# Kernel tuning notes

Measured on AMD Instinct MI355X. Metric: run time of the kernel, lower is better.

## Reference

```python
import jax, jax.numpy as jnp
from jax import lax
import numpy as np

B, H, N, F = 8, 512, 64, 256
P = 12  # prediction_steps


def setup_inputs() -> dict:
    key = jax.random.key(0)
    ks = jax.random.split(key, 6)
    s_in = 1.0 / np.sqrt(N * F)
    s_f = 1.0 / np.sqrt(F)
    return {
        "x": jax.random.normal(ks[0], (B, H, N, F), jnp.float32),
        "W1": jax.random.normal(ks[1], (N * F, F), jnp.float32) * s_in,
        "b1": jnp.zeros((F,), jnp.float32),
        "Wx": jax.random.normal(ks[2], (F, 4 * F), jnp.float32) * s_f,
        "Wh": jax.random.normal(ks[3], (F, 4 * F), jnp.float32) * s_f,
        "b": jnp.zeros((4 * F,), jnp.float32),
        "Wa": jax.random.normal(ks[4], (F, F), jnp.float32) * s_f,
        "ba": jnp.zeros((F,), jnp.float32),
        "W2": jax.random.normal(ks[5], (F, N), jnp.float32) * s_f,
        "b2": jnp.zeros((N,), jnp.float32),
    }


def _lstm_cell(h, c, xt, Wx, Wh, b):
    # Keras LSTMCell gate order: i, f, g(candidate), o
    z = xt @ Wx + h @ Wh + b  # (B, 4F)
    i, f, g, o = jnp.split(z, 4, axis=-1)
    c_new = jax.nn.sigmoid(f) * c + jax.nn.sigmoid(i) * jnp.tanh(g)
    h_new = jax.nn.sigmoid(o) * jnp.tanh(c_new)
    return h_new, c_new


def reference(x, W1, b1, Wx, Wh, b, Wa, ba, W2, b2):
    Bx, Hx, Nx, Fx = x.shape
    xs = x.reshape(Bx, Hx, Nx * Fx) @ W1 + b1  # dense1: (B,H,F)

    def enc_step(carry, xt):
        h, c = carry
        h, c = _lstm_cell(h, c, xt, Wx, Wh, b)
        return (h, c), h

    h0 = jnp.zeros((Bx, Fx), x.dtype)
    (h, c), enc = lax.scan(enc_step, (h0, h0), jnp.swapaxes(xs, 0, 1))
    enc = jnp.swapaxes(enc, 0, 1)  # encoder_states (B,H,F)

    def dec_step(carry, _):
        h, c, mem = carry
        q = mem @ Wa + ba                          # (B,F)
        scores = jnp.einsum('bf,bhf->bh', q, enc)  # dot-product attention
        w = jax.nn.softmax(scores, axis=-1)
        ctx = jnp.einsum('bh,bhf->bf', w, enc)
        h, c = _lstm_cell(h, c, ctx, Wx, Wh, b)
        return (h, c, h), h

    (_, _, _), preds = lax.scan(dec_step, (h, c, h), None, length=P)
    preds = jnp.swapaxes(preds, 0, 1)  # (B,P,F)
    return preds @ W2 + b2  # (B,P,N)
```

## Files before the change

### kernel.cpp

```cpp
#include <hip/hip_runtime.h>
#include <hip/hip_bf16.h>
#include <stdint.h>

#define B_ 8
#define H_ 512
#define F_ 256
#define P_ 12
#define M_ 4096
#define K1_ 16384
#define J_ 1024

typedef __attribute__((ext_vector_type(8))) short short8;
typedef __attribute__((ext_vector_type(4))) float floatx4;

union FragU { uint4 u; short8 s; };

#define OFF_W1H   ((size_t)0)
#define OFF_W1L   ((size_t)8388608)
#define OFF_WHSW  ((size_t)16777216)
#define OFF_ENC   ((size_t)17301504)
#define OFF_C     ((size_t)21495808)
#define OFF_XSUM  ((size_t)21504000)
#define OFF_XPRE  ((size_t)25698304)
#define OFF_P1    ((size_t)42475520)
#define OFF_ENCT  (OFF_P1)
#define OFF_HST   (OFF_P1 + (size_t)4194304)
#define OFF_CTXG  (OFF_HST + (size_t)8192)
#define OFF_ZG    (OFF_CTXG + (size_t)8192)

__device__ __forceinline__ unsigned short f2bf(float f) {
  uint32_t u = __float_as_uint(f);
  u += 0x7fffu + ((u >> 16) & 1u);
  return (unsigned short)(u >> 16);
}
__device__ __forceinline__ float bf2f(unsigned short h) {
  return __uint_as_float(((uint32_t)h) << 16);
}
__device__ __forceinline__ float sigm(float x) { return 1.f / (1.f + __expf(-x)); }
__device__ __forceinline__ float tanh_(float x) {
  float ax = fabsf(x);
  float e  = __expf(-2.f * ax);
  float t  = (1.f - e) / (1.f + e);
  return x < 0.f ? -t : t;
}

__global__ void k_prep_w1(const float* __restrict__ W1,
                          uint4* __restrict__ hi, uint4* __restrict__ lo) {
  int idx  = blockIdx.x * 1024 + threadIdx.x;
  int lane = idx & 63;
  int kt   = (idx >> 6) & 511;
  int nt   = idx >> 15;
  int n    = nt * 16 + (lane & 15);
  int kb   = kt * 32 + ((lane >> 4) << 3);
  unsigned short h8[8], l8[8];
#pragma unroll
  for (int j = 0; j < 8; ++j) {
    float v = W1[(size_t)(kb + j) * 256 + n];
    unsigned short hh = f2bf(v);
    h8[j] = hh;
    l8[j] = f2bf(v - bf2f(hh));
  }
  uint4 uh, ul;
  uh.x = (uint32_t)h8[0] | ((uint32_t)h8[1] << 16);
  uh.y = (uint32_t)h8[2] | ((uint32_t)h8[3] << 16);
  uh.z = (uint32_t)h8[4] | ((uint32_t)h8[5] << 16);
  uh.w = (uint32_t)h8[6] | ((uint32_t)h8[7] << 16);
  ul.x = (uint32_t)l8[0] | ((uint32_t)l8[1] << 16);
  ul.y = (uint32_t)l8[2] | ((uint32_t)l8[3] << 16);
  ul.z = (uint32_t)l8[4] | ((uint32_t)l8[5] << 16);
  ul.w = (uint32_t)l8[6] | ((uint32_t)l8[7] << 16);
  hi[idx] = uh;
  lo[idx] = ul;
}

__global__ void k_prep_wh(const float* __restrict__ Wh, uint4* __restrict__ sw) {
  int idx  = blockIdx.x * 1024 + threadIdx.x;
  int lane = idx & 63;
  int kt   = (idx >> 6) & 7;
  int zt   = idx >> 9;
  int col  = zt * 16 + (lane & 15);
  int kb   = kt * 32 + ((lane >> 4) << 3);
  unsigned short h8[8];
#pragma unroll
  for (int j = 0; j < 8; ++j) h8[j] = f2bf(Wh[(size_t)(kb + j) * 1024 + col]);
  uint4 u;
  u.x = (uint32_t)h8[0] | ((uint32_t)h8[1] << 16);
  u.y = (uint32_t)h8[2] | ((uint32_t)h8[3] << 16);
  u.z = (uint32_t)h8[4] | ((uint32_t)h8[5] << 16);
  u.w = (uint32_t)h8[6] | ((uint32_t)h8[7] << 16);
  sw[idx] = u;
}

__global__ __launch_bounds__(1024)
void k_gemm1(const float* __restrict__ x, const uint4* __restrict__ w1h,
             const uint4* __restrict__ w1l, float* __restrict__ P1) {
  __shared__ __align__(16) unsigned short xh[128 * 40];
  __shared__ __align__(16) unsigned short xl[128 * 40];
  int bm = blockIdx.x >> 3, kc = blockIdx.x & 7;
  int m0 = bm * 128, kcbase = kc * 2048;
  int tid = threadIdx.x, wave = tid >> 6, lane = tid & 63;
  int quad = lane >> 4, l15 = lane & 15;
  int srow = tid >> 3, skch = tid & 7;
  floatx4 acc[8];
#pragma unroll
  for (int mt = 0; mt < 8; ++mt) acc[mt] = (floatx4)(0.f);

  const float* xrow = x + (size_t)(m0 + srow) * K1_ + kcbase + skch * 4;
  float4 xv = *(const float4*)(xrow);
  for (int it = 0; it < 64; ++it) {
    unsigned short h0 = f2bf(xv.x), h1 = f2bf(xv.y), h2 = f2bf(xv.z), h3 = f2bf(xv.w);
    unsigned short g0 = f2bf(xv.x - bf2f(h0)), g1 = f2bf(xv.y - bf2f(h1));
    unsigned short g2 = f2bf(xv.z - bf2f(h2)), g3 = f2bf(xv.w - bf2f(h3));
    uint2 ph, pl;
    ph.x = (uint32_t)h0 | ((uint32_t)h1 << 16); ph.y = (uint32_t)h2 | ((uint32_t)h3 << 16);
    pl.x = (uint32_t)g0 | ((uint32_t)g1 << 16); pl.y = (uint32_t)g2 | ((uint32_t)g3 << 16);
    *(uint2*)&xh[srow * 40 + skch * 4] = ph;
    *(uint2*)&xl[srow * 40 + skch * 4] = pl;
    __syncthreads();

    float4 xn = xv;
    if (it < 63) xn = *(const float4*)(xrow + (it + 1) * 32);

    size_t aoff = (size_t)(wave * 512 + kc * 64 + it) * 64 + lane;
    FragU ah; ah.u = w1h[aoff];
    FragU al; al.u = w1l[aoff];
#pragma unroll
    for (int mt = 0; mt < 8; ++mt) {
      FragU bh, bl;
      bh.u = *(const uint4*)&xh[(mt * 16 + l15) * 40 + quad * 8];
      bl.u = *(const uint4*)&xl[(mt * 16 + l15) * 40 + quad * 8];
      acc[mt] = __builtin_amdgcn_mfma_f32_16x16x32_bf16(ah.s, bh.s, acc[mt], 0, 0, 0);
      acc[mt] = __builtin_amdgcn_mfma_f32_16x16x32_bf16(ah.s, bl.s, acc[mt], 0, 0, 0);
      acc[mt] = __builtin_amdgcn_mfma_f32_16x16x32_bf16(al.s, bh.s, acc[mt], 0, 0, 0);
    }
    __syncthreads();
    xv = xn;
  }
  int nbase = wave * 16 + quad * 4;
#pragma unroll
  for (int mt = 0; mt < 8; ++mt) {
    int m = m0 + mt * 16 + l15;
#pragma unroll
    for (int r = 0; r < 4; ++r)
      P1[(size_t)(kc * 256 + nbase + r) * M_ + m] = acc[mt][r];
  }
}

__global__ void k_reduce(const float* __restrict__ P1, const float* __restrict__ b1,
                         float* __restrict__ xsum) {
  int idx = blockIdx.x * 1024 + threadIdx.x;
  int k = idx >> 12, m = idx & 4095;
  float s = b1[k];
#pragma unroll
  for (int kc = 0; kc < 8; ++kc) s += P1[(size_t)(kc * 256 + k) * M_ + m];
  xsum[(size_t)k * M_ + m] = s;
}

__global__ __launch_bounds__(256)
void k_gemm2(const float* __restrict__ xsum, const float* __restrict__ Wx,
             const float* __restrict__ bz, float* __restrict__ Xpre) {
  int m0 = blockIdx.x * 16;
  int j = threadIdx.x;
  float acc0[16], acc1[16], acc2[16], acc3[16];
  float bb0 = bz[j], bb1 = bz[256 + j], bb2 = bz[512 + j], bb3 = bz[768 + j];
#pragma unroll
  for (int mm = 0; mm < 16; ++mm) { acc0[mm] = bb0; acc1[mm] = bb1; acc2[mm] = bb2; acc3[mm] = bb3; }
#pragma unroll 4
  for (int k = 0; k < 256; ++k) {
    float w0 = Wx[(size_t)k * 1024 + j];
    float w1 = Wx[(size_t)k * 1024 + 256 + j];
    float w2 = Wx[(size_t)k * 1024 + 512 + j];
    float w3 = Wx[(size_t)k * 1024 + 768 + j];
#pragma unroll
    for (int mm = 0; mm < 16; ++mm) {
      float xv = xsum[(size_t)k * M_ + m0 + mm];
      acc0[mm] += xv * w0; acc1[mm] += xv * w1; acc2[mm] += xv * w2; acc3[mm] += xv * w3;
    }
  }
#pragma unroll
  for (int mm = 0; mm < 16; ++mm) {
    float* o = Xpre + (size_t)(m0 + mm) * 1024;
    o[j] = acc0[mm]; o[256 + j] = acc1[mm]; o[512 + j] = acc2[mm]; o[768 + j] = acc3[mm];
  }
}

__global__ __launch_bounds__(512, 2)
void k_encoder(const uint4* __restrict__ whsw, const float* __restrict__ Xpre,
               float* __restrict__ enc, float* __restrict__ encT,
               float* __restrict__ cws) {
  __shared__ uint4 wl[8192];
  __shared__ __align__(16) unsigned short hb[2][512];
  __shared__ __align__(16) float zsh[2048];
  int b = blockIdx.x, tid = threadIdx.x;
  int wave = tid >> 6, lane = tid & 63;
  int quad = lane >> 4, l15 = lane & 15;
  int e = tid & 1, j = tid >> 1;

  for (int r = 0; r < 16; ++r) {
    int u = r * 512 + tid;
    int ln = u & 63, fr = u >> 6;
    int w = fr >> 4, G = (fr >> 3) & 1, kt = fr & 7;
    int zt = 16 * (2 * G + 1) + 2 * w + 1;
    wl[u] = whsw[(size_t)((zt * 8 + kt) * 64 + ln)];
  }
  uint4 wfr[48];
#pragma unroll
  for (int G = 0; G < 2; ++G)
#pragma unroll
    for (int i = 0; i < 3; ++i) {
      int zt = 16 * (2 * G + (i >> 1)) + 2 * wave + (i & 1);
#pragma unroll
      for (int kt = 0; kt < 8; ++kt)
        wfr[(G * 3 + i) * 8 + kt] = whsw[(size_t)((zt * 8 + kt) * 64 + lane)];
    }

  hb[0][tid] = 0; hb[1][tid] = 0;
  float c_ = 0.f;
  const float* xpb = Xpre + (size_t)b * 512 * 1024;
  int colA = 256 * e + j;
  int colB = 512 + colA;
  int hoff  = ((l15 == 1) ? 256 : 0) + quad * 8;
  int zwoff = ((l15 == 1) ? 1024 : 0) + quad * 4;
  __syncthreads();

  int cur = 0;
  for (int t = 0; t < 512; ++t) {
    const unsigned short* hbc = hb[cur];
    float xA = xpb[(size_t)t * 1024 + colA];
    float xB = xpb[(size_t)t * 1024 + colB];

#pragma unroll
    for (int G = 0; G < 2; ++G) {
      const uint4* wlg = wl + (size_t)((wave * 2 + G) * 8) * 64 + lane;
      FragU bfr[8], pfr[8];
#pragma unroll
      for (int k = 0; k < 3; ++k) {
        bfr[k].u = *(const uint4*)&hbc[hoff + k * 32];
        pfr[k].u = wlg[(size_t)k * 64];
      }
      floatx4 a0 = (floatx4)(0.f), a1 = (floatx4)(0.f);
      floatx4 a2 = (floatx4)(0.f), a3 = (floatx4)(0.f);
#pragma unroll
      for (int kt = 0; kt < 8; ++kt) {
        if (kt < 5) {
          bfr[kt + 3].u = *(const uint4*)&hbc[hoff + (kt + 3) * 32];
          pfr[kt + 3].u = wlg[(size_t)(kt + 3) * 64];
        }
        FragU f0, f1, f2;
        f0.u = wfr[(G * 3 + 0) * 8 + kt];
        f1.u = wfr[(G * 3 + 1) * 8 + kt];
        f2.u = wfr[(G * 3 + 2) * 8 + kt];
        a0 = __builtin_amdgcn_mfma_f32_16x16x32_bf16(f0.s, bfr[kt].s, a0, 0, 0, 0);
        a1 = __builtin_amdgcn_mfma_f32_16x16x32_bf16(f1.s, bfr[kt].s, a1, 0, 0, 0);
        a2 = __builtin_amdgcn_mfma_f32_16x16x32_bf16(f2.s, bfr[kt].s, a2, 0, 0, 0);
        a3 = __builtin_amdgcn_mfma_f32_16x16x32_bf16(pfr[kt].s, bfr[kt].s, a3, 0, 0, 0);
      }
      if (l15 < 2) {
        int zt0 = 16 * (2 * G) + 2 * wave;
        int zt2 = 16 * (2 * G + 1) + 2 * wave;
        *(floatx4*)&zsh[zwoff + zt0 * 16]        = a0;
        *(floatx4*)&zsh[zwoff + (zt0 + 1) * 16]  = a1;
        *(floatx4*)&zsh[zwoff + zt2 * 16]        = a2;
        *(floatx4*)&zsh[zwoff + (zt2 + 1) * 16]  = a3;
      }
    }

    float zA = zsh[colA] + zsh[1024 + colA] + xA;
    float zB = zsh[colB] + zsh[1024 + colB] + xB;
    float actA = sigm(zA);
    float tnh = tanh_(zB), sg = sigm(zB);
    float actB = e ? sg : tnh;
    float p = actA * actB;
    float send = e ? actA : p;
    float recv = __shfl_xor(send, 1, 64);
    float cn = e ? (actA * c_ + recv)
                 : (recv * c_ + p);
    c_ = cn;
    float th = tanh_(cn);
    float hn = actB * th;
    int nxt = cur ^ 1;
    if (e) {
      enc[((size_t)b * 512 + t) * 256 + j] = hn;
      encT[((size_t)b * 256 + j) * 512 + t] = hn;
      unsigned short hh = f2bf(hn);
      hb[nxt][j] = hh;
      hb[nxt][256 + j] = f2bf(hn - bf2f(hh));
    }
    __syncthreads();
    cur = nxt;
  }
  if (e) cws[b * 256 + j] = c_;
}

__global__ __launch_bounds__(1024)
void k_dec_att(const float* __restrict__ enc, const float* __restrict__ encT,
               float* __restrict__ hst, float* __restrict__ cst,
               const float* __restrict__ zg, float* __restrict__ ctxg,
               const float* __restrict__ Wa, const float* __restrict__ ba,
               const float* __restrict__ W2, const float* __restrict__ b2,
               float* __restrict__ out, int p) {
  __shared__ float hsh[256], qsh[256], sc[512], smx[2];
  __shared__ float zb[1024];
  int b = blockIdx.x, tid = threadIdx.x;
  const float* encb = enc + (size_t)b * 512 * 256;

  if (p > 0) {
    if (tid < 256) {
      float zi = zg[b * 1024 + tid];
      float zf = zg[b * 1024 + 256 + tid];
      float zgg = zg[b * 1024 + 512 + tid];
      float zo = zg[b * 1024 + 768 + tid];
      float ig = sigm(zi), fg = sigm(zf), gg = tanh_(zgg), og = sigm(zo);
      float cn = fg * cst[b * 256 + tid] + ig * gg;
      cst[b * 256 + tid] = cn;
      float hn = og * tanh_(cn);
      hsh[tid] = hn;
      hst[b * 256 + tid] = hn;
    }
    __syncthreads();
    {
      if (tid < 512) {
        int col = tid & 63, kc = tid >> 6;
        float s = 0.f;
#pragma unroll
        for (int i = 0; i < 32; ++i) {
          int k = kc * 32 + i;
          s += hsh[k] * W2[(size_t)k * 64 + col];
        }
        zb[tid] = s;
      }
    }
    __syncthreads();
    if (tid < 64) {
      float s = b2[tid];
#pragma unroll
      for (int kc = 0; kc < 8; ++kc) s += zb[kc * 64 + tid];
      out[((size_t)b * 12 + (p - 1)) * 64 + tid] = s;
    }
  } else {
    if (tid < 256) {
      float hv = encb[(size_t)511 * 256 + tid];
      hsh[tid] = hv;
      hst[b * 256 + tid] = hv;
    }
  }
  if (p == 12) return;
  __syncthreads();

  {
    int j = tid & 255, kc = tid >> 8;
    float s = 0.f;
#pragma unroll 8
    for (int i = 0; i < 64; ++i) {
      int k = kc * 64 + i;
      s += hsh[k] * Wa[(size_t)k * 256 + j];
    }
    zb[tid] = s;
  }
  __syncthreads();
  if (tid < 256) qsh[tid] = ba[tid] + zb[tid] + zb[256 + tid] + zb[512 + tid] + zb[768 + tid];
  __syncthreads();

  {
    int hh = tid & 511, kc = tid >> 9;
    const float* eT = encT + (size_t)b * 256 * 512;
    float s = 0.f;
#pragma unroll 8
    for (int i = 0; i < 128; ++i) {
      int k = kc * 128 + i;
      s += qsh[k] * eT[(size_t)k * 512 + hh];
    }
    zb[tid] = s;
  }
  __syncthreads();
  if (tid < 512) sc[tid] = zb[tid] + zb[512 + tid];
  __syncthreads();

  if (tid < 64) {
    float m = -3.4e38f;
#pragma unroll
    for (int r = 0; r < 8; ++r) m = fmaxf(m, sc[tid * 8 + r]);
#pragma unroll
    for (int off = 32; off >= 1; off >>= 1) m = fmaxf(m, __shfl_xor(m, off, 64));
    if (tid == 0) smx[0] = m;
  }
  __syncthreads();
  if (tid < 512) sc[tid] = __expf(sc[tid] - smx[0]);
  __syncthreads();
  if (tid < 64) {
    float s = 0.f;
#pragma unroll
    for (int r = 0; r < 8; ++r) s += sc[tid * 8 + r];
#pragma unroll
    for (int off = 32; off >= 1; off >>= 1) s += __shfl_xor(s, off, 64);
    if (tid == 0) smx[1] = 1.f / s;
  }
  __syncthreads();

  {
    int j = tid & 255, hs = tid >> 8;
    float s = 0.f;
#pragma unroll 8
    for (int r = 0; r < 128; ++r) {
      int hh = hs * 128 + r;
      s += sc[hh] * encb[(size_t)hh * 256 + j];
    }
    zb[tid] = s;
  }
  __syncthreads();
  if (tid < 256)
    ctxg[b * 256 + tid] = (zb[tid] + zb[256 + tid] + zb[512 + tid] + zb[768 + tid]) * smx[1];
}

__global__ __launch_bounds__(512)
void k_dec_z(const float* __restrict__ ctxg, const float* __restrict__ hst,
             const float* __restrict__ Wx, const float* __restrict__ Wh,
             const float* __restrict__ bz, float* __restrict__ zg) {
  __shared__ float ldsx[256], ldsh[256], zsh[512];
  int chunk = blockIdx.x & 7, b = blockIdx.x >> 3;
  int tid = threadIdx.x;
  int j = tid & 127, ks = (tid >> 7) & 1, sel = tid >> 8;
  int col = chunk * 128 + j;

  if (tid < 256) ldsx[tid] = ctxg[b * 256 + tid];
  else ldsh[tid - 256] = hst[b * 256 + (tid - 256)];
  __syncthreads();

  const float* W = sel ? Wh : Wx;
  const float* v = sel ? ldsh : ldsx;
  float s = 0.f;
#pragma unroll 8
  for (int i = 0; i < 128; ++i) {
    int k = ks * 128 + i;
    s += v[k] * W[(size_t)k * 1024 + col];
  }
  zsh[tid] = s;
  __syncthreads();
  if (tid < 128)
    zg[b * 1024 + col] = bz[col] + zsh[j] + zsh[128 + j] + zsh[256 + j] + zsh[384 + j];
}

extern "C" void kernel_launch(void* const* d_in, const int* in_sizes, int n_in,
                              void* d_out, int out_size, void* d_ws, size_t ws_size,
                              hipStream_t stream) {
  const float* x  = (const float*)d_in[0];
  const float* W1 = (const float*)d_in[1];
  const float* b1 = (const float*)d_in[2];
  const float* Wx = (const float*)d_in[3];
  const float* Wh = (const float*)d_in[4];
  const float* bz = (const float*)d_in[5];
  const float* Wa = (const float*)d_in[6];
  const float* ba = (const float*)d_in[7];
  const float* W2 = (const float*)d_in[8];
  const float* b2 = (const float*)d_in[9];

  char* ws = (char*)d_ws;
  uint4* w1h  = (uint4*)(ws + OFF_W1H);
  uint4* w1l  = (uint4*)(ws + OFF_W1L);
  uint4* whsw = (uint4*)(ws + OFF_WHSW);
  float* enc  = (float*)(ws + OFF_ENC);
  float* cws  = (float*)(ws + OFF_C);
  float* xsum = (float*)(ws + OFF_XSUM);
  float* xpre = (float*)(ws + OFF_XPRE);
  float* p1   = (float*)(ws + OFF_P1);
  float* encT = (float*)(ws + OFF_ENCT);
  float* hst  = (float*)(ws + OFF_HST);
  float* ctxg = (float*)(ws + OFF_CTXG);
  float* zg   = (float*)(ws + OFF_ZG);

  k_prep_w1<<<dim3(512), dim3(1024), 0, stream>>>(W1, w1h, w1l);
  k_prep_wh<<<dim3(32), dim3(1024), 0, stream>>>(Wh, whsw);
  k_gemm1<<<dim3(256), dim3(1024), 0, stream>>>(x, w1h, w1l, p1);
  k_reduce<<<dim3(1024), dim3(1024), 0, stream>>>(p1, b1, xsum);
  k_gemm2<<<dim3(256), dim3(256), 0, stream>>>(xsum, Wx, bz, xpre);
  k_encoder<<<dim3(8), dim3(512), 0, stream>>>(whsw, xpre, enc, encT, cws);
  for (int p = 0; p <= 12; ++p) {
    k_dec_att<<<dim3(8), dim3(1024), 0, stream>>>(enc, encT, hst, cws, zg, ctxg,
                                                  Wa, ba, W2, b2, (float*)d_out, p);
    if (p < 12)
      k_dec_z<<<dim3(64), dim3(512), 0, stream>>>(ctxg, hst, Wx, Wh, bz, zg);
  }
}
```

Before: 1.989 ms.

## Fuse decoder gate GEMV into attention kernel and rebalance encoder weight residency

The decoder's separate z-projection kernel is folded into the attention step kernel, so each step computes ctx and the Wx/Wh gate preactivations in one launch. This halves decoder launches and drops the global round-trips for h and ctx. The cost is that the gate GEMV now runs on only 8 blocks instead of 64. Separately, the encoder reshuffles which Wh fragments live in registers (46) versus LDS (18 per wave) and restructures the MFMA loops into two groups of four accumulators, using explicit waves-per-EU attributes.

Measured after the change: 1.942 ms. -2.4%, faster.

```diff
diff --git a/kernel.cpp b/kernel.cpp
--- a/kernel.cpp
+++ b/kernel.cpp
@@ -24,9 +24,7 @@
 #define OFF_XPRE  ((size_t)25698304)
 #define OFF_P1    ((size_t)42475520)
 #define OFF_ENCT  (OFF_P1)
-#define OFF_HST   (OFF_P1 + (size_t)4194304)
-#define OFF_CTXG  (OFF_HST + (size_t)8192)
-#define OFF_ZG    (OFF_CTXG + (size_t)8192)
+#define OFF_ZG    (OFF_ENCT + (size_t)4194304)
 
 __device__ __forceinline__ unsigned short f2bf(float f) {
   uint32_t u = __float_as_uint(f);
@@ -184,11 +182,12 @@
   }
 }
 
-__global__ __launch_bounds__(512, 2)
+__global__ __attribute__((amdgpu_flat_work_group_size(512, 512)))
+__attribute__((amdgpu_waves_per_eu(2, 2)))
 void k_encoder(const uint4* __restrict__ whsw, const float* __restrict__ Xpre,
                float* __restrict__ enc, float* __restrict__ encT,
                float* __restrict__ cws) {
-  __shared__ uint4 wl[8192];
+  __shared__ uint4 wl[9216];
   __shared__ __align__(16) unsigned short hb[2][512];
   __shared__ __align__(16) float zsh[2048];
   int b = blockIdx.x, tid = threadIdx.x;
@@ -196,23 +195,30 @@
   int quad = lane >> 4, l15 = lane & 15;
   int e = tid & 1, j = tid >> 1;
 
-  for (int r = 0; r < 16; ++r) {
+  for (int r = 0; r < 18; ++r) {
     int u = r * 512 + tid;
-    int ln = u & 63, fr = u >> 6;
-    int w = fr >> 4, G = (fr >> 3) & 1, kt = fr & 7;
-    int zt = 16 * (2 * G + 1) + 2 * w + 1;
+    int ln = u & 63, fslot = u >> 6;
+    int w = fslot / 18, fi = fslot - w * 18;
+    int i = (fi < 8) ? 6 : ((fi < 16) ? 7 : 5);
+    int kt = (fi < 8) ? fi : ((fi < 16) ? fi - 8 : fi - 10);
+    int zt = 16 * (i >> 1) + 2 * w + (i & 1);
     wl[u] = whsw[(size_t)((zt * 8 + kt) * 64 + ln)];
   }
-  uint4 wfr[48];
-#pragma unroll
-  for (int G = 0; G < 2; ++G)
-#pragma unroll
-    for (int i = 0; i < 3; ++i) {
-      int zt = 16 * (2 * G + (i >> 1)) + 2 * wave + (i & 1);
-#pragma unroll
-      for (int kt = 0; kt < 8; ++kt)
-        wfr[(G * 3 + i) * 8 + kt] = whsw[(size_t)((zt * 8 + kt) * 64 + lane)];
-    }
+
+  uint4 wfr[46];
+#pragma unroll
+  for (int i = 0; i < 5; ++i) {
+    int zt = 16 * (i >> 1) + 2 * wave + (i & 1);
+#pragma unroll
+    for (int kt = 0; kt < 8; ++kt)
+      wfr[i * 8 + kt] = whsw[(size_t)((zt * 8 + kt) * 64 + lane)];
+  }
+  {
+    int zt = 33 + 2 * wave;
+#pragma unroll
+    for (int kt = 0; kt < 6; ++kt)
+      wfr[40 + kt] = whsw[(size_t)((zt * 8 + kt) * 64 + lane)];
+  }
 
   hb[0][tid] = 0; hb[1][tid] = 0;
   float c_ = 0.f;
@@ -221,6 +227,7 @@
   int colB = 512 + colA;
   int hoff  = ((l15 == 1) ? 256 : 0) + quad * 8;
   int zwoff = ((l15 == 1) ? 1024 : 0) + quad * 4;
+  const uint4* wlw = wl + (size_t)(wave * 18) * 64 + lane;
   __syncthreads();
 
   int cur = 0;
@@ -229,39 +236,67 @@
     float xA = xpb[(size_t)t * 1024 + colA];
     float xB = xpb[(size_t)t * 1024 + colB];
 
-#pragma unroll
-    for (int G = 0; G < 2; ++G) {
-      const uint4* wlg = wl + (size_t)((wave * 2 + G) * 8) * 64 + lane;
-      FragU bfr[8], pfr[8];
-#pragma unroll
-      for (int k = 0; k < 3; ++k) {
-        bfr[k].u = *(const uint4*)&hbc[hoff + k * 32];
-        pfr[k].u = wlg[(size_t)k * 64];
-      }
+    {
       floatx4 a0 = (floatx4)(0.f), a1 = (floatx4)(0.f);
       floatx4 a2 = (floatx4)(0.f), a3 = (floatx4)(0.f);
+      FragU bf; bf.u = *(const uint4*)&hbc[hoff];
 #pragma unroll
       for (int kt = 0; kt < 8; ++kt) {
-        if (kt < 5) {
-          bfr[kt + 3].u = *(const uint4*)&hbc[hoff + (kt + 3) * 32];
-          pfr[kt + 3].u = wlg[(size_t)(kt + 3) * 64];
-        }
-        FragU f0, f1, f2;
-        f0.u = wfr[(G * 3 + 0) * 8 + kt];
-        f1.u = wfr[(G * 3 + 1) * 8 + kt];
-        f2.u = wfr[(G * 3 + 2) * 8 + kt];
-        a0 = __builtin_amdgcn_mfma_f32_16x16x32_bf16(f0.s, bfr[kt].s, a0, 0, 0, 0);
-        a1 = __builtin_amdgcn_mfma_f32_16x16x32_bf16(f1.s, bfr[kt].s, a1, 0, 0, 0);
-        a2 = __builtin_amdgcn_mfma_f32_16x16x32_bf16(f2.s, bfr[kt].s, a2, 0, 0, 0);
-        a3 = __builtin_amdgcn_mfma_f32_16x16x32_bf16(pfr[kt].s, bfr[kt].s, a3, 0, 0, 0);
+        FragU bfn;
+        if (kt < 7) bfn.u = *(const uint4*)&hbc[hoff + (kt + 1) * 32];
+        FragU f0, f1, f2, f3;
+        f0.u = wfr[0 + kt];  f1.u = wfr[8 + kt];
+        f2.u = wfr[16 + kt]; f3.u = wfr[24 + kt];
+        a0 = __builtin_amdgcn_mfma_f32_16x16x32_bf16(f0.s, bf.s, a0, 0, 0, 0);
+        a1 = __builtin_amdgcn_mfma_f32_16x16x32_bf16(f1.s, bf.s, a1, 0, 0, 0);
+        a2 = __builtin_amdgcn_mfma_f32_16x16x32_bf16(f2.s, bf.s, a2, 0, 0, 0);
+        a3 = __builtin_amdgcn_mfma_f32_16x16x32_bf16(f3.s, bf.s, a3, 0, 0, 0);
+        if (kt < 7) bf = bfn;
       }
       if (l15 < 2) {
-        int zt0 = 16 * (2 * G) + 2 * wave;
-        int zt2 = 16 * (2 * G + 1) + 2 * wave;
-        *(floatx4*)&zsh[zwoff + zt0 * 16]        = a0;
-        *(floatx4*)&zsh[zwoff + (zt0 + 1) * 16]  = a1;
-        *(floatx4*)&zsh[zwoff + zt2 * 16]        = a2;
-        *(floatx4*)&zsh[zwoff + (zt2 + 1) * 16]  = a3;
+        *(floatx4*)&zsh[zwoff + (2 * wave) * 16]      = a0;
+        *(floatx4*)&zsh[zwoff + (2 * wave + 1) * 16]  = a1;
+        *(floatx4*)&zsh[zwoff + (16 + 2 * wave) * 16] = a2;
+        *(floatx4*)&zsh[zwoff + (17 + 2 * wave) * 16] = a3;
+      }
+    }
+    {
+      floatx4 a4 = (floatx4)(0.f), a5 = (floatx4)(0.f);
+      floatx4 a6 = (floatx4)(0.f), a7 = (floatx4)(0.f);
+      FragU p5a, p5b;
+      p5a.u = wlw[(size_t)16 * 64];
+      p5b.u = wlw[(size_t)17 * 64];
+      FragU bf, p6, p7;
+      bf.u = *(const uint4*)&hbc[hoff];
+      p6.u = wlw[0];
+      p7.u = wlw[(size_t)8 * 64];
+#pragma unroll
+      for (int kt = 0; kt < 8; ++kt) {
+        FragU bfn, p6n, p7n;
+        if (kt < 7) {
+          bfn.u = *(const uint4*)&hbc[hoff + (kt + 1) * 32];
+          p6n.u = wlw[(size_t)(kt + 1) * 64];
+          p7n.u = wlw[(size_t)(9 + kt) * 64];
+        }
+        FragU f4; f4.u = wfr[32 + kt];
+        a4 = __builtin_amdgcn_mfma_f32_16x16x32_bf16(f4.s, bf.s, a4, 0, 0, 0);
+        if (kt < 6) {
+          FragU f5; f5.u = wfr[40 + kt];
+          a5 = __builtin_amdgcn_mfma_f32_16x16x32_bf16(f5.s, bf.s, a5, 0, 0, 0);
+        } else if (kt == 6) {
+          a5 = __builtin_amdgcn_mfma_f32_16x16x32_bf16(p5a.s, bf.s, a5, 0, 0, 0);
+        } else {
+          a5 = __builtin_amdgcn_mfma_f32_16x16x32_bf16(p5b.s, bf.s, a5, 0, 0, 0);
+        }
+        a6 = __builtin_amdgcn_mfma_f32_16x16x32_bf16(p6.s, bf.s, a6, 0, 0, 0);
+        a7 = __builtin_amdgcn_mfma_f32_16x16x32_bf16(p7.s, bf.s, a7, 0, 0, 0);
+        if (kt < 7) { bf = bfn; p6 = p6n; p7 = p7n; }
+      }
+      if (l15 < 2) {
+        *(floatx4*)&zsh[zwoff + (32 + 2 * wave) * 16] = a4;
+        *(floatx4*)&zsh[zwoff + (33 + 2 * wave) * 16] = a5;
+        *(floatx4*)&zsh[zwoff + (48 + 2 * wave) * 16] = a6;
+        *(floatx4*)&zsh[zwoff + (49 + 2 * wave) * 16] = a7;
       }
     }
 
@@ -293,13 +328,14 @@
 }
 
 __global__ __launch_bounds__(1024)
-void k_dec_att(const float* __restrict__ enc, const float* __restrict__ encT,
-               float* __restrict__ hst, float* __restrict__ cst,
-               const float* __restrict__ zg, float* __restrict__ ctxg,
-               const float* __restrict__ Wa, const float* __restrict__ ba,
-               const float* __restrict__ W2, const float* __restrict__ b2,
-               float* __restrict__ out, int p) {
-  __shared__ float hsh[256], qsh[256], sc[512], smx[2];
+void k_dec_step(const float* __restrict__ enc, const float* __restrict__ encT,
+                float* __restrict__ cst, float* __restrict__ zg,
+                const float* __restrict__ Wx, const float* __restrict__ Wh,
+                const float* __restrict__ bz,
+                const float* __restrict__ Wa, const float* __restrict__ ba,
+                const float* __restrict__ W2, const float* __restrict__ b2,
+                float* __restrict__ out, int p) {
+  __shared__ float hsh[256], qsh[256], ctxs[256], sc[512], smx[2];
   __shared__ float zb[1024];
   int b = blockIdx.x, tid = threadIdx.x;
   const float* encb = enc + (size_t)b * 512 * 256;
@@ -313,22 +349,18 @@
       float ig = sigm(zi), fg = sigm(zf), gg = tanh_(zgg), og = sigm(zo);
       float cn = fg * cst[b * 256 + tid] + ig * gg;
       cst[b * 256 + tid] = cn;
-      float hn = og * tanh_(cn);
-      hsh[tid] = hn;
-      hst[b * 256 + tid] = hn;
+      hsh[tid] = og * tanh_(cn);
     }
     __syncthreads();
-    {
-      if (tid < 512) {
-        int col = tid & 63, kc = tid >> 6;
-        float s = 0.f;
-#pragma unroll
-        for (int i = 0; i < 32; ++i) {
-          int k = kc * 32 + i;
-          s += hsh[k] * W2[(size_t)k * 64 + col];
-        }
-        zb[tid] = s;
+    if (tid < 512) {
+      int col = tid & 63, kc = tid >> 6;
+      float s = 0.f;
+#pragma unroll
+      for (int i = 0; i < 32; ++i) {
+        int k = kc * 32 + i;
+        s += hsh[k] * W2[(size_t)k * 64 + col];
       }
+      zb[tid] = s;
     }
     __syncthreads();
     if (tid < 64) {
@@ -338,22 +370,18 @@
       out[((size_t)b * 12 + (p - 1)) * 64 + tid] = s;
     }
   } else {
-    if (tid < 256) {
-      float hv = encb[(size_t)511 * 256 + tid];
-      hsh[tid] = hv;
-      hst[b * 256 + tid] = hv;
-    }
+    if (tid < 256) hsh[tid] = encb[(size_t)511 * 256 + tid];
   }
   if (p == 12) return;
   __syncthreads();
 
   {
-    int j = tid & 255, kc = tid >> 8;
+    int jj = tid & 255, kc = tid >> 8;
     float s = 0.f;
 #pragma unroll 8
     for (int i = 0; i < 64; ++i) {
       int k = kc * 64 + i;
-      s += hsh[k] * Wa[(size_t)k * 256 + j];
+      s += hsh[k] * Wa[(size_t)k * 256 + jj];
     }
     zb[tid] = s;
   }
@@ -398,46 +426,27 @@
   __syncthreads();
 
   {
-    int j = tid & 255, hs = tid >> 8;
+    int jj = tid & 255, hs = tid >> 8;
     float s = 0.f;
 #pragma unroll 8
     for (int r = 0; r < 128; ++r) {
       int hh = hs * 128 + r;
-      s += sc[hh] * encb[(size_t)hh * 256 + j];
+      s += sc[hh] * encb[(size_t)hh * 256 + jj];
     }
     zb[tid] = s;
   }
   __syncthreads();
   if (tid < 256)
-    ctxg[b * 256 + tid] = (zb[tid] + zb[256 + tid] + zb[512 + tid] + zb[768 + tid]) * smx[1];
-}
-
-__global__ __launch_bounds__(512)
-void k_dec_z(const float* __restrict__ ctxg, const float* __restrict__ hst,
-             const float* __restrict__ Wx, const float* __restrict__ Wh,
-             const float* __restrict__ bz, float* __restrict__ zg) {
-  __shared__ float ldsx[256], ldsh[256], zsh[512];
-  int chunk = blockIdx.x & 7, b = blockIdx.x >> 3;
-  int tid = threadIdx.x;
-  int j = tid & 127, ks = (tid >> 7) & 1, sel = tid >> 8;
-  int col = chunk * 128 + j;
-
-  if (tid < 256) ldsx[tid] = ctxg[b * 256 + tid];
-  else ldsh[tid - 256] = hst[b * 256 + (tid - 256)];
-  __syncthreads();
-
-  const float* W = sel ? Wh : Wx;
-  const float* v = sel ? ldsh : ldsx;
-  float s = 0.f;
-#pragma unroll 8
-  for (int i = 0; i < 128; ++i) {
-    int k = ks * 128 + i;
-    s += v[k] * W[(size_t)k * 1024 + col];
-  }
-  zsh[tid] = s;
-  __syncthreads();
-  if (tid < 128)
-    zg[b * 1024 + col] = bz[col] + zsh[j] + zsh[128 + j] + zsh[256 + j] + zsh[384 + j];
+    ctxs[tid] = (zb[tid] + zb[256 + tid] + zb[512 + tid] + zb[768 + tid]) * smx[1];
+  __syncthreads();
+
+  {
+    float s = bz[tid];
+#pragma unroll 16
+    for (int k = 0; k < 256; ++k)
+      s += ctxs[k] * Wx[(size_t)k * 1024 + tid] + hsh[k] * Wh[(size_t)k * 1024 + tid];
+    zg[b * 1024 + tid] = s;
+  }
 }
 
 extern "C" void kernel_launch(void* const* d_in, const int* in_sizes, int n_in,
@@ -464,8 +473,6 @@
   float* xpre = (float*)(ws + OFF_XPRE);
   float* p1   = (float*)(ws + OFF_P1);
   float* encT = (float*)(ws + OFF_ENCT);
-  float* hst  = (float*)(ws + OFF_HST);
-  float* ctxg = (float*)(ws + OFF_CTXG);
   float* zg   = (float*)(ws + OFF_ZG);
 
   k_prep_w1<<<dim3(512), dim3(1024), 0, stream>>>(W1, w1h, w1l);
@@ -474,10 +481,8 @@
   k_reduce<<<dim3(1024), dim3(1024), 0, stream>>>(p1, b1, xsum);
   k_gemm2<<<dim3(256), dim3(256), 0, stream>>>(xsum, Wx, bz, xpre);
   k_encoder<<<dim3(8), dim3(512), 0, stream>>>(whsw, xpre, enc, encT, cws);
-  for (int p = 0; p <= 12; ++p) {
-    k_dec_att<<<dim3(8), dim3(1024), 0, stream>>>(enc, encT, hst, cws, zg, ctxg,
-                                                  Wa, ba, W2, b2, (float*)d_out, p);
-    if (p < 12)
-      k_dec_z<<<dim3(64), dim3(512), 0, stream>>>(ctxg, hst, Wx, Wh, bz, zg);
-  }
-}
+  for (int p = 0; p <= 12; ++p)
+    k_dec_step<<<dim3(8), dim3(1024), 0, stream>>>(enc, encT, cws, zg,
+                                                   Wx, Wh, bz, Wa, ba, W2, b2,
+                                                   (float*)d_out, p);
+}
```

## Restructure LSTM encoder step so each wave owns full gate columns in registers

Applied to the files above, without the earlier changes.

The encoder recurrence now has each wave compute all four gates for its own 32 hidden units with eight MFMA accumulators, covering the 16 output columns of a 16x16 tile. It combines the hi/lo bf16 halves with a lane shuffle instead of writing partial sums to shared memory and rereading them after a barrier, which removes one shared round-trip per timestep. Weight fragments are redistributed between registers (46 uint4) and a larger LDS buffer. The next timestep's input projection is prefetched into a double-buffered shared tile. This shortens the serial per-step critical path, at the cost of higher register pressure and fewer active lanes doing the gate math and stores.

Result: slower. 4.717 ms (+137.2%).

```diff
diff --git a/kernel.cpp b/kernel.cpp
--- a/kernel.cpp
+++ b/kernel.cpp
@@ -184,112 +184,163 @@
   }
 }
 
-__global__ __launch_bounds__(512, 2)
+__global__ __attribute__((amdgpu_flat_work_group_size(512, 512)))
+__attribute__((amdgpu_waves_per_eu(2, 2)))
 void k_encoder(const uint4* __restrict__ whsw, const float* __restrict__ Xpre,
                float* __restrict__ enc, float* __restrict__ encT,
                float* __restrict__ cws) {
-  __shared__ uint4 wl[8192];
+  __shared__ uint4 wl[9216];
   __shared__ __align__(16) unsigned short hb[2][512];
-  __shared__ __align__(16) float zsh[2048];
+  __shared__ __align__(16) float xst[2][1024];
   int b = blockIdx.x, tid = threadIdx.x;
   int wave = tid >> 6, lane = tid & 63;
   int quad = lane >> 4, l15 = lane & 15;
-  int e = tid & 1, j = tid >> 1;
-
-  for (int r = 0; r < 16; ++r) {
+
+  for (int r = 0; r < 18; ++r) {
     int u = r * 512 + tid;
-    int ln = u & 63, fr = u >> 6;
-    int w = fr >> 4, G = (fr >> 3) & 1, kt = fr & 7;
-    int zt = 16 * (2 * G + 1) + 2 * w + 1;
+    int ln = u & 63, fslot = u >> 6;
+    int w = fslot / 18, fi = fslot - w * 18;
+    int i = (fi < 8) ? 6 : ((fi < 16) ? 7 : 5);
+    int kt = (fi < 8) ? fi : ((fi < 16) ? fi - 8 : fi - 10);
+    int zt = 16 * (i >> 1) + 2 * w + (i & 1);
     wl[u] = whsw[(size_t)((zt * 8 + kt) * 64 + ln)];
   }
-  uint4 wfr[48];
-#pragma unroll
-  for (int G = 0; G < 2; ++G)
-#pragma unroll
-    for (int i = 0; i < 3; ++i) {
-      int zt = 16 * (2 * G + (i >> 1)) + 2 * wave + (i & 1);
-#pragma unroll
-      for (int kt = 0; kt < 8; ++kt)
-        wfr[(G * 3 + i) * 8 + kt] = whsw[(size_t)((zt * 8 + kt) * 64 + lane)];
-    }
+
+  uint4 wfr[46];
+#pragma unroll
+  for (int i = 0; i < 5; ++i) {
+    int zt = 16 * (i >> 1) + 2 * wave + (i & 1);
+#pragma unroll
+    for (int kt = 0; kt < 8; ++kt)
+      wfr[i * 8 + kt] = whsw[(size_t)((zt * 8 + kt) * 64 + lane)];
+  }
+  {
+    int zt = 33 + 2 * wave;
+#pragma unroll
+    for (int kt = 0; kt < 6; ++kt)
+      wfr[40 + kt] = whsw[(size_t)((zt * 8 + kt) * 64 + lane)];
+  }
 
   hb[0][tid] = 0; hb[1][tid] = 0;
-  float c_ = 0.f;
+  float cr[8];
+#pragma unroll
+  for (int u = 0; u < 8; ++u) cr[u] = 0.f;
   const float* xpb = Xpre + (size_t)b * 512 * 1024;
-  int colA = 256 * e + j;
-  int colB = 512 + colA;
-  int hoff  = ((l15 == 1) ? 256 : 0) + quad * 8;
-  int zwoff = ((l15 == 1) ? 1024 : 0) + quad * 4;
+  { float2 v = *(const float2*)(xpb + 2 * tid); *(float2*)&xst[0][2 * tid] = v; }
+  int hoff = ((l15 == 1) ? 256 : 0) + quad * 8;
+  const uint4* wlw = wl + (size_t)(wave * 18) * 64 + lane;
+  int jb = 32 * wave + 4 * quad;
   __syncthreads();
 
   int cur = 0;
   for (int t = 0; t < 512; ++t) {
     const unsigned short* hbc = hb[cur];
-    float xA = xpb[(size_t)t * 1024 + colA];
-    float xB = xpb[(size_t)t * 1024 + colB];
-
-#pragma unroll
-    for (int G = 0; G < 2; ++G) {
-      const uint4* wlg = wl + (size_t)((wave * 2 + G) * 8) * 64 + lane;
-      FragU bfr[8], pfr[8];
-#pragma unroll
-      for (int k = 0; k < 3; ++k) {
-        bfr[k].u = *(const uint4*)&hbc[hoff + k * 32];
-        pfr[k].u = wlg[(size_t)k * 64];
+    float2 xnext;
+    if (t < 511) xnext = *(const float2*)(xpb + (size_t)(t + 1) * 1024 + 2 * tid);
+
+    floatx4 a0 = (floatx4)(0.f), a1 = (floatx4)(0.f);
+    floatx4 a2 = (floatx4)(0.f), a3 = (floatx4)(0.f);
+    floatx4 a4 = (floatx4)(0.f), a5 = (floatx4)(0.f);
+    floatx4 a6 = (floatx4)(0.f), a7 = (floatx4)(0.f);
+#pragma unroll
+    for (int kt = 0; kt < 8; ++kt) {
+      FragU bf; bf.u = *(const uint4*)&hbc[hoff + kt * 32];
+      FragU w0_, w1_, w2_, w3_, w4_, w5_, w6_, w7_;
+      w0_.u = wfr[0 + kt];  w1_.u = wfr[8 + kt];
+      w2_.u = wfr[16 + kt]; w3_.u = wfr[24 + kt];
+      w4_.u = wfr[32 + kt];
+      w5_.u = (kt < 6) ? wfr[40 + kt] : wlw[(size_t)(16 + (kt - 6)) * 64];
+      w6_.u = wlw[(size_t)kt * 64];
+      w7_.u = wlw[(size_t)(8 + kt) * 64];
+      a0 = __builtin_amdgcn_mfma_f32_16x16x32_bf16(w0_.s, bf.s, a0, 0, 0, 0);
+      a1 = __builtin_amdgcn_mfma_f32_16x16x32_bf16(w1_.s, bf.s, a1, 0, 0, 0);
+      a2 = __builtin_amdgcn_mfma_f32_16x16x32_bf16(w2_.s, bf.s, a2, 0, 0, 0);
+      a3 = __builtin_amdgcn_mfma_f32_16x16x32_bf16(w3_.s, bf.s, a3, 0, 0, 0);
+      a4 = __builtin_amdgcn_mfma_f32_16x16x32_bf16(w4_.s, bf.s, a4, 0, 0, 0);
+      a5 = __builtin_amdgcn_mfma_f32_16x16x32_bf16(w5_.s, bf.s, a5, 0, 0, 0);
+      a6 = __builtin_amdgcn_mfma_f32_16x16x32_bf16(w6_.s, bf.s, a6, 0, 0, 0);
+      a7 = __builtin_amdgcn_mfma_f32_16x16x32_bf16(w7_.s, bf.s, a7, 0, 0, 0);
+    }
+
+#define COMB(Z, A) floatx4 Z; { \
+  _Pragma("unroll") for (int r_ = 0; r_ < 4; ++r_) \
+    Z[r_] = A[r_] + __shfl_xor(A[r_], 1, 64); }
+    COMB(za0, a0) COMB(za1, a1) COMB(za2, a2) COMB(za3, a3)
+    COMB(za4, a4) COMB(za5, a5) COMB(za6, a6) COMB(za7, a7)
+#undef COMB
+
+    const float* xc = xst[cur];
+    floatx4 xi0 = *(const floatx4*)&xc[jb];
+    floatx4 xf0 = *(const floatx4*)&xc[256 + jb];
+    floatx4 xg0 = *(const floatx4*)&xc[512 + jb];
+    floatx4 xo0 = *(const floatx4*)&xc[768 + jb];
+    floatx4 xi1 = *(const floatx4*)&xc[16 + jb];
+    floatx4 xf1 = *(const floatx4*)&xc[272 + jb];
+    floatx4 xg1 = *(const floatx4*)&xc[528 + jb];
+    floatx4 xo1 = *(const floatx4*)&xc[784 + jb];
+    float hn[8];
+#define GATEBLK(HF, ZI, ZF, ZG, ZO, XI, XF, XG, XO) { \
+  _Pragma("unroll") for (int r_ = 0; r_ < 4; ++r_) { \
+    float zi = ZI[r_] + XI[r_]; \
+    float zf = ZF[r_] + XF[r_]; \
+    float zg = ZG[r_] + XG[r_]; \
+    float zo = ZO[r_] + XO[r_]; \
+    float ig = sigm(zi), fg = sigm(zf); \
+    float gg = tanh_(zg), og = sigm(zo); \
+    float cn = fg * cr[(HF) * 4 + r_] + ig * gg; \
+    cr[(HF) * 4 + r_] = cn; \
+    hn[(HF) * 4 + r_] = og * tanh_(cn); } }
+    GATEBLK(0, za0, za2, za4, za6, xi0, xf0, xg0, xo0)
+    GATEBLK(1, za1, za3, za5, za7, xi1, xf1, xg1, xo1)
+#undef GATEBLK
+
+    int nxt = cur ^ 1;
+    unsigned short* hbn = hb[nxt];
+    if (l15 == 0) {
+      unsigned short hi8[8], lo8[8];
+#pragma unroll
+      for (int u = 0; u < 8; ++u) {
+        unsigned short hh = f2bf(hn[u]);
+        hi8[u] = hh;
+        lo8[u] = f2bf(hn[u] - bf2f(hh));
       }
-      floatx4 a0 = (floatx4)(0.f), a1 = (floatx4)(0.f);
-      floatx4 a2 = (floatx4)(0.f), a3 = (floatx4)(0.f);
-#pragma unroll
-      for (int kt = 0; kt < 8; ++kt) {
-        if (kt < 5) {
-          bfr[kt + 3].u = *(const uint4*)&hbc[hoff + (kt + 3) * 32];
-          pfr[kt + 3].u = wlg[(size_t)(kt + 3) * 64];
-        }
-        FragU f0, f1, f2;
-        f0.u = wfr[(G * 3 + 0) * 8 + kt];
-        f1.u = wfr[(G * 3 + 1) * 8 + kt];
-        f2.u = wfr[(G * 3 + 2) * 8 + kt];
-        a0 = __builtin_amdgcn_mfma_f32_16x16x32_bf16(f0.s, bfr[kt].s, a0, 0, 0, 0);
-        a1 = __builtin_amdgcn_mfma_f32_16x16x32_bf16(f1.s, bfr[kt].s, a1, 0, 0, 0);
-        a2 = __builtin_amdgcn_mfma_f32_16x16x32_bf16(f2.s, bfr[kt].s, a2, 0, 0, 0);
-        a3 = __builtin_amdgcn_mfma_f32_16x16x32_bf16(pfr[kt].s, bfr[kt].s, a3, 0, 0, 0);
+      uint2 w0, w1;
+      w0.x = (uint32_t)hi8[0] | ((uint32_t)hi8[1] << 16);
+      w0.y = (uint32_t)hi8[2] | ((uint32_t)hi8[3] << 16);
+      w1.x = (uint32_t)hi8[4] | ((uint32_t)hi8[5] << 16);
+      w1.y = (uint32_t)hi8[6] | ((uint32_t)hi8[7] << 16);
+      *(uint2*)&hbn[jb] = w0;
+      *(uint2*)&hbn[16 + jb] = w1;
+      w0.x = (uint32_t)lo8[0] | ((uint32_t)lo8[1] << 16);
+      w0.y = (uint32_t)lo8[2] | ((uint32_t)lo8[3] << 16);
+      w1.x = (uint32_t)lo8[4] | ((uint32_t)lo8[5] << 16);
+      w1.y = (uint32_t)lo8[6] | ((uint32_t)lo8[7] << 16);
+      *(uint2*)&hbn[256 + jb] = w0;
+      *(uint2*)&hbn[272 + jb] = w1;
+      float* encrow = enc + ((size_t)b * 512 + t) * 256;
+      floatx4 e0, e1;
+      e0[0] = hn[0]; e0[1] = hn[1]; e0[2] = hn[2]; e0[3] = hn[3];
+      e1[0] = hn[4]; e1[1] = hn[5]; e1[2] = hn[6]; e1[3] = hn[7];
+      *(floatx4*)&encrow[jb] = e0;
+      *(floatx4*)&encrow[16 + jb] = e1;
+      float* eTb = encT + (size_t)b * 256 * 512 + t;
+#pragma unroll
+      for (int r = 0; r < 4; ++r) {
+        eTb[(size_t)(jb + r) * 512] = hn[r];
+        eTb[(size_t)(jb + 16 + r) * 512] = hn[4 + r];
       }
-      if (l15 < 2) {
-        int zt0 = 16 * (2 * G) + 2 * wave;
-        int zt2 = 16 * (2 * G + 1) + 2 * wave;
-        *(floatx4*)&zsh[zwoff + zt0 * 16]        = a0;
-        *(floatx4*)&zsh[zwoff + (zt0 + 1) * 16]  = a1;
-        *(floatx4*)&zsh[zwoff + zt2 * 16]        = a2;
-        *(floatx4*)&zsh[zwoff + (zt2 + 1) * 16]  = a3;
-      }
-    }
-
-    float zA = zsh[colA] + zsh[1024 + colA] + xA;
-    float zB = zsh[colB] + zsh[1024 + colB] + xB;
-    float actA = sigm(zA);
-    float tnh = tanh_(zB), sg = sigm(zB);
-    float actB = e ? sg : tnh;
-    float p = actA * actB;
-    float send = e ? actA : p;
-    float recv = __shfl_xor(send, 1, 64);
-    float cn = e ? (actA * c_ + recv)
-                 : (recv * c_ + p);
-    c_ = cn;
-    float th = tanh_(cn);
-    float hn = actB * th;
-    int nxt = cur ^ 1;
-    if (e) {
-      enc[((size_t)b * 512 + t) * 256 + j] = hn;
-      encT[((size_t)b * 256 + j) * 512 + t] = hn;
-      unsigned short hh = f2bf(hn);
-      hb[nxt][j] = hh;
-      hb[nxt][256 + j] = f2bf(hn - bf2f(hh));
-    }
+    }
+    if (t < 511) *(float2*)&xst[nxt][2 * tid] = xnext;
     __syncthreads();
     cur = nxt;
   }
-  if (e) cws[b * 256 + j] = c_;
+  if (l15 == 0) {
+#pragma unroll
+    for (int r = 0; r < 4; ++r) {
+      cws[b * 256 + jb + r] = cr[r];
+      cws[b * 256 + jb + 16 + r] = cr[4 + r];
+    }
+  }
 }
 
 __global__ __launch_bounds__(1024)
@@ -318,17 +369,15 @@
       hst[b * 256 + tid] = hn;
     }
     __syncthreads();
-    {
-      if (tid < 512) {
-        int col = tid & 63, kc = tid >> 6;
-        float s = 0.f;
-#pragma unroll
-        for (int i = 0; i < 32; ++i) {
-          int k = kc * 32 + i;
-          s += hsh[k] * W2[(size_t)k * 64 + col];
-        }
-        zb[tid] = s;
+    if (tid < 512) {
+      int col = tid & 63, kc = tid >> 6;
+      float s = 0.f;
+#pragma unroll
+      for (int i = 0; i < 32; ++i) {
+        int k = kc * 32 + i;
+        s += hsh[k] * W2[(size_t)k * 64 + col];
       }
+      zb[tid] = s;
     }
     __syncthreads();
     if (tid < 64) {
```

## Split encoder recurrent matmul across 16 waves with 1024-thread blocks

Applied to the files above, without the earlier changes.

The sequential LSTM encoder kernel now runs 1024 threads per block (16 waves) instead of 512, so each wave computes one z-tile group per gate instead of two. This halves per-wave MFMA work on the critical serial path and halves register-held weight fragments. The cost is a second barrier per timestep, since pointwise gate math stays on the first 512 threads and must wait for all waves' z results. Half the threads now idle during the activation phase.

Result: slower. 2.534 ms (+27.4%).

```diff
diff --git a/kernel.cpp b/kernel.cpp
--- a/kernel.cpp
+++ b/kernel.cpp
@@ -184,7 +184,7 @@
   }
 }
 
-__global__ __launch_bounds__(512, 2)
+__global__ __attribute__((amdgpu_flat_work_group_size(1024, 1024)))
 void k_encoder(const uint4* __restrict__ whsw, const float* __restrict__ Xpre,
                float* __restrict__ enc, float* __restrict__ encT,
                float* __restrict__ cws) {
@@ -196,100 +196,91 @@
   int quad = lane >> 4, l15 = lane & 15;
   int e = tid & 1, j = tid >> 1;
 
-  for (int r = 0; r < 16; ++r) {
-    int u = r * 512 + tid;
-    int ln = u & 63, fr = u >> 6;
-    int w = fr >> 4, G = (fr >> 3) & 1, kt = fr & 7;
-    int zt = 16 * (2 * G + 1) + 2 * w + 1;
-    wl[u] = whsw[(size_t)((zt * 8 + kt) * 64 + ln)];
-  }
-  uint4 wfr[48];
-#pragma unroll
-  for (int G = 0; G < 2; ++G)
-#pragma unroll
-    for (int i = 0; i < 3; ++i) {
-      int zt = 16 * (2 * G + (i >> 1)) + 2 * wave + (i & 1);
-#pragma unroll
-      for (int kt = 0; kt < 8; ++kt)
-        wfr[(G * 3 + i) * 8 + kt] = whsw[(size_t)((zt * 8 + kt) * 64 + lane)];
-    }
-
-  hb[0][tid] = 0; hb[1][tid] = 0;
+  for (int r = 0; r < 8; ++r) {
+    int u = r * 1024 + tid;
+    int ln = u & 63, fslot = u >> 6;
+    int w = fslot >> 3, kt = fslot & 7;
+    wl[u] = whsw[(size_t)(((48 + w) * 8 + kt) * 64 + ln)];
+  }
+
+  uint4 wfr[24];
+#pragma unroll
+  for (int g = 0; g < 3; ++g) {
+    int zt = 16 * g + wave;
+#pragma unroll
+    for (int kt = 0; kt < 8; ++kt)
+      wfr[g * 8 + kt] = whsw[(size_t)((zt * 8 + kt) * 64 + lane)];
+  }
+
+  if (tid < 512) { hb[0][tid] = 0; hb[1][tid] = 0; }
   float c_ = 0.f;
   const float* xpb = Xpre + (size_t)b * 512 * 1024;
   int colA = 256 * e + j;
   int colB = 512 + colA;
   int hoff  = ((l15 == 1) ? 256 : 0) + quad * 8;
   int zwoff = ((l15 == 1) ? 1024 : 0) + quad * 4;
+  const uint4* wlw = wl + (size_t)(wave * 8) * 64 + lane;
   __syncthreads();
 
   int cur = 0;
   for (int t = 0; t < 512; ++t) {
     const unsigned short* hbc = hb[cur];
-    float xA = xpb[(size_t)t * 1024 + colA];
-    float xB = xpb[(size_t)t * 1024 + colB];
-
-#pragma unroll
-    for (int G = 0; G < 2; ++G) {
-      const uint4* wlg = wl + (size_t)((wave * 2 + G) * 8) * 64 + lane;
-      FragU bfr[8], pfr[8];
-#pragma unroll
-      for (int k = 0; k < 3; ++k) {
-        bfr[k].u = *(const uint4*)&hbc[hoff + k * 32];
-        pfr[k].u = wlg[(size_t)k * 64];
+    float xA = 0.f, xB = 0.f;
+    if (tid < 512) {
+      xA = xpb[(size_t)t * 1024 + colA];
+      xB = xpb[(size_t)t * 1024 + colB];
+    }
+
+    floatx4 a0 = (floatx4)(0.f), a1 = (floatx4)(0.f);
+    floatx4 a2 = (floatx4)(0.f), a3 = (floatx4)(0.f);
+#pragma unroll
+    for (int kt = 0; kt < 8; ++kt) {
+      FragU bf; bf.u = *(const uint4*)&hbc[hoff + kt * 32];
+      FragU f0, f1, f2, p3;
+      f0.u = wfr[0 + kt];
+      f1.u = wfr[8 + kt];
+      f2.u = wfr[16 + kt];
+      p3.u = wlw[(size_t)kt * 64];
+      a0 = __builtin_amdgcn_mfma_f32_16x16x32_bf16(f0.s, bf.s, a0, 0, 0, 0);
+      a1 = __builtin_amdgcn_mfma_f32_16x16x32_bf16(f1.s, bf.s, a1, 0, 0, 0);
+      a2 = __builtin_amdgcn_mfma_f32_16x16x32_bf16(f2.s, bf.s, a2, 0, 0, 0);
+      a3 = __builtin_amdgcn_mfma_f32_16x16x32_bf16(p3.s, bf.s, a3, 0, 0, 0);
+    }
+    if (l15 < 2) {
+      *(floatx4*)&zsh[zwoff +       16 * wave] = a0;
+      *(floatx4*)&zsh[zwoff + 256 + 16 * wave] = a1;
+      *(floatx4*)&zsh[zwoff + 512 + 16 * wave] = a2;
+      *(floatx4*)&zsh[zwoff + 768 + 16 * wave] = a3;
+    }
+    __syncthreads();
+
+    int nxt = cur ^ 1;
+    if (tid < 512) {
+      float zA = zsh[colA] + zsh[1024 + colA] + xA;
+      float zB = zsh[colB] + zsh[1024 + colB] + xB;
+      float actA = sigm(zA);
+      float tnh = tanh_(zB), sg = sigm(zB);
+      float actB = e ? sg : tnh;
+      float p = actA * actB;
+      float send = e ? actA : p;
+      float recv = __shfl_xor(send, 1, 64);
+      float cn = e ? (actA * c_ + recv)
+                   : (recv * c_ + p);
+      c_ = cn;
+      float th = tanh_(cn);
+      float hn = actB * th;
+      if (e) {
+        enc[((size_t)b * 512 + t) * 256 + j] = hn;
+        encT[((size_t)b * 256 + j) * 512 + t] = hn;
+        unsigned short hh = f2bf(hn);
+        hb[nxt][j] = hh;
+        hb[nxt][256 + j] = f2bf(hn - bf2f(hh));
       }
-      floatx4 a0 = (floatx4)(0.f), a1 = (floatx4)(0.f);
-      floatx4 a2 = (floatx4)(0.f), a3 = (floatx4)(0.f);
-#pragma unroll
-      for (int kt = 0; kt < 8; ++kt) {
-        if (kt < 5) {
-          bfr[kt + 3].u = *(const uint4*)&hbc[hoff + (kt + 3) * 32];
-          pfr[kt + 3].u = wlg[(size_t)(kt + 3) * 64];
-        }
-        FragU f0, f1, f2;
-        f0.u = wfr[(G * 3 + 0) * 8 + kt];
-        f1.u = wfr[(G * 3 + 1) * 8 + kt];
-        f2.u = wfr[(G * 3 + 2) * 8 + kt];
-        a0 = __builtin_amdgcn_mfma_f32_16x16x32_bf16(f0.s, bfr[kt].s, a0, 0, 0, 0);
-        a1 = __builtin_amdgcn_mfma_f32_16x16x32_bf16(f1.s, bfr[kt].s, a1, 0, 0, 0);
-        a2 = __builtin_amdgcn_mfma_f32_16x16x32_bf16(f2.s, bfr[kt].s, a2, 0, 0, 0);
-        a3 = __builtin_amdgcn_mfma_f32_16x16x32_bf16(pfr[kt].s, bfr[kt].s, a3, 0, 0, 0);
-      }
-      if (l15 < 2) {
-        int zt0 = 16 * (2 * G) + 2 * wave;
-        int zt2 = 16 * (2 * G + 1) + 2 * wave;
-        *(floatx4*)&zsh[zwoff + zt0 * 16]        = a0;
-        *(floatx4*)&zsh[zwoff + (zt0 + 1) * 16]  = a1;
-        *(floatx4*)&zsh[zwoff + zt2 * 16]        = a2;
-        *(floatx4*)&zsh[zwoff + (zt2 + 1) * 16]  = a3;
-      }
-    }
-
-    float zA = zsh[colA] + zsh[1024 + colA] + xA;
-    float zB = zsh[colB] + zsh[1024 + colB] + xB;
-    float actA = sigm(zA);
-    float tnh = tanh_(zB), sg = sigm(zB);
-    float actB = e ? sg : tnh;
-    float p = actA * actB;
-    float send = e ? actA : p;
-    float recv = __shfl_xor(send, 1, 64);
-    float cn = e ? (actA * c_ + recv)
-                 : (recv * c_ + p);
-    c_ = cn;
-    float th = tanh_(cn);
-    float hn = actB * th;
-    int nxt = cur ^ 1;
-    if (e) {
-      enc[((size_t)b * 512 + t) * 256 + j] = hn;
-      encT[((size_t)b * 256 + j) * 512 + t] = hn;
-      unsigned short hh = f2bf(hn);
-      hb[nxt][j] = hh;
-      hb[nxt][256 + j] = f2bf(hn - bf2f(hh));
     }
     __syncthreads();
     cur = nxt;
   }
-  if (e) cws[b * 256 + j] = c_;
+  if (tid < 512 && e) cws[b * 256 + j] = c_;
 }
 
 __global__ __launch_bounds__(1024)
@@ -318,17 +309,15 @@
       hst[b * 256 + tid] = hn;
     }
     __syncthreads();
-    {
-      if (tid < 512) {
-        int col = tid & 63, kc = tid >> 6;
-        float s = 0.f;
-#pragma unroll
-        for (int i = 0; i < 32; ++i) {
-          int k = kc * 32 + i;
-          s += hsh[k] * W2[(size_t)k * 64 + col];
-        }
-        zb[tid] = s;
+    if (tid < 512) {
+      int col = tid & 63, kc = tid >> 6;
+      float s = 0.f;
+#pragma unroll
+      for (int i = 0; i < 32; ++i) {
+        int k = kc * 32 + i;
+        s += hsh[k] * W2[(size_t)k * 64 + col];
       }
+      zb[tid] = s;
     }
     __syncthreads();
     if (tid < 64) {
@@ -473,7 +462,7 @@
   k_gemm1<<<dim3(256), dim3(1024), 0, stream>>>(x, w1h, w1l, p1);
   k_reduce<<<dim3(1024), dim3(1024), 0, stream>>>(p1, b1, xsum);
   k_gemm2<<<dim3(256), dim3(256), 0, stream>>>(xsum, Wx, bz, xpre);
-  k_encoder<<<dim3(8), dim3(512), 0, stream>>>(whsw, xpre, enc, encT, cws);
+  k_encoder<<<dim3(8), dim3(1024), 0, stream>>>(whsw, xpre, enc, encT, cws);
   for (int p = 0; p <= 12; ++p) {
     k_dec_att<<<dim3(8), dim3(1024), 0, stream>>>(enc, encT, hst, cws, zg, ctxg,
                                                   Wa, ba, W2, b2, (float*)d_out, p);
```
